# Kernel tuning notes

Hardware: AMD Instinct MI355X
Metric: run time of the kernel (lower is better)

The kernel has to match this reference:

```python
import jax, jax.numpy as jnp
import numpy as np

B, L, D, H = 2, 4096, 768, 12
HS = D // H  # head_size = 64
SCALE = HS ** -0.5


def setup_inputs() -> dict:
    key = jax.random.key(0)
    k1, k2, k3 = jax.random.split(key, 3)
    x = jax.random.normal(k1, (B, L, D), dtype=jnp.float32)
    # torch nn.Linear weights are [out_features, in_features]; y = x @ W.T
    Wq = jax.random.normal(k2, (D, D), dtype=jnp.float32) * (D ** -0.5)
    Wo = jax.random.normal(k3, (D, D), dtype=jnp.float32) * (D ** -0.5)
    return {"x": x, "Wq": Wq, "Wo": Wo}


def reference(x, Wq, Wo):
    b, l, d = x.shape
    # NOTE: source module uses self.query for Q, K, AND V (bug preserved).
    q = jnp.einsum('bld,ed->ble', x, Wq)              # [B,L,D]
    q = q.reshape(b, l, H, HS).transpose(0, 2, 1, 3)   # [B,H,L,HS]
    k = v = q                                          # K = V = Q (faithful)
    scores = jnp.einsum('bhqd,bhkd->bhqk', q, k) * SCALE  # [B,H,L,L]
    attn = jax.nn.softmax(scores, axis=-1)
    out = jnp.einsum('bhqk,bhkd->bhqd', attn, v)       # [B,H,L,HS]
    out = out.transpose(0, 2, 1, 3).reshape(b, l, d)   # [B,L,D]
    out = jnp.einsum('bld,ed->ble', out, Wo)           # output projection
    return out
```

## Files before the change

kernel.cpp:

```cpp
#include <hip/hip_runtime.h>
#include <hip/hip_bf16.h>

#define LQ 4096
#define DQ 768
#define NH 12
#define NB 2

typedef __attribute__((ext_vector_type(8))) short short8;
typedef __attribute__((ext_vector_type(2))) unsigned uint2v;
typedef __attribute__((ext_vector_type(4))) float f32x4;

__device__ __forceinline__ short f2bf(float f) {
    union { float f; unsigned u; } v; v.f = f;
    unsigned r = v.u + 0x7FFFu + ((v.u >> 16) & 1u);
    return (short)(r >> 16);
}

__device__ __forceinline__ unsigned pk2(float a, float b) {
    float2 t; t.x = a; t.y = b;
    __hip_bfloat162 h = __float22bfloat162_rn(t);
    unsigned u; __builtin_memcpy(&u, &h, 4);
    return u;
}

__device__ __forceinline__ f32x4 mfma16(short8 a, short8 b, f32x4 c) {
    return __builtin_amdgcn_mfma_f32_16x16x32_bf16(a, b, c, 0, 0, 0);
}

__device__ __forceinline__ void gld16(const short* g, short* l) {
    __builtin_amdgcn_global_load_lds(
        (const __attribute__((address_space(1))) unsigned int*)(g),
        (__attribute__((address_space(3))) unsigned int*)(l), 16, 0, 0);
}

#define SQRT_C 0.424660891f

__global__ __launch_bounds__(256) void cvtw(const float* __restrict__ a,
                                            short* __restrict__ o) {
    int i = blockIdx.x * 256 + threadIdx.x;
    float4 v = ((const float4*)a)[i];
    *(uint2v*)&o[i * 4] = (uint2v){pk2(v.x, v.y), pk2(v.z, v.w)};
}


template <int MODE>
__global__ __launch_bounds__(256, 3) void gemm_nt(const short* __restrict__ A,
                                                  const short* __restrict__ Wb,
                                                  void* __restrict__ Cp,
                                                  short* __restrict__ Vf) {
    __shared__ __attribute__((aligned(16))) short As[2][128 * 64];
    __shared__ __attribute__((aligned(16))) short Bs[2][64 * 64];
    const int t = threadIdx.x;
    const int lane = t & 63, w = t >> 6;
    const int lr = lane & 15, qd = lane >> 4;
    const int wm = (w & 1) * 64, wn = (w >> 1) * 32;
    const int lin = blockIdx.x;
    const int xcd = lin & 7, jj = lin >> 3;
    const int nt = jj % 12, mt = (jj / 12) * 8 + xcd;
    const int m0 = mt * 128, n0 = nt * 64;

    int aoffs[4], boffs[2];
#pragma unroll
    for (int u = 0; u < 4; ++u) {
        int c = (u * 4 + w) * 64 + lane;
        int row = c >> 3, k = (c & 7) ^ (row & 7);
        aoffs[u] = (m0 + row) * DQ + k * 8;
    }
#pragma unroll
    for (int u = 0; u < 2; ++u) {
        int c = (u * 4 + w) * 64 + lane;
        int row = c >> 3, k = (c & 7) ^ (row & 7);
        boffs[u] = (n0 + row) * DQ + k * 8;
    }

    f32x4 acc[4][2];
#pragma unroll
    for (int i = 0; i < 4; ++i)
#pragma unroll
        for (int j = 0; j < 2; ++j) acc[i][j] = (f32x4){0.f, 0.f, 0.f, 0.f};

#pragma unroll
    for (int u = 0; u < 4; ++u) gld16(&A[aoffs[u]], &As[0][(u * 4 + w) * 512]);
#pragma unroll
    for (int u = 0; u < 2; ++u) gld16(&Wb[boffs[u]], &Bs[0][(u * 4 + w) * 512]);
    __syncthreads();

    int cur = 0;
    for (int kt = 0; kt < 12; ++kt) {
        if (kt < 11) {
            const int k0 = (kt + 1) * 64;
#pragma unroll
            for (int u = 0; u < 4; ++u) gld16(&A[aoffs[u] + k0], &As[cur ^ 1][(u * 4 + w) * 512]);
#pragma unroll
            for (int u = 0; u < 2; ++u) gld16(&Wb[boffs[u] + k0], &Bs[cur ^ 1][(u * 4 + w) * 512]);
        }
#pragma unroll
        for (int s = 0; s < 2; ++s) {
            const int cq = ((4 * s + qd) ^ (lr & 7)) * 8;
            short8 af[4], bf[2];
#pragma unroll
            for (int i = 0; i < 4; ++i)
                af[i] = *(short8*)&As[cur][(wm + 16 * i + lr) * 64 + cq];
#pragma unroll
            for (int j = 0; j < 2; ++j)
                bf[j] = *(short8*)&Bs[cur][(wn + 16 * j + lr) * 64 + cq];
#pragma unroll
            for (int i = 0; i < 4; ++i)
#pragma unroll
                for (int j = 0; j < 2; ++j)
                    acc[i][j] = mfma16(af[i], bf[j], acc[i][j]);
        }
        __syncthreads();
        cur ^= 1;
    }

    if (MODE == 0) {
#pragma unroll
        for (int i = 0; i < 4; ++i)
#pragma unroll
            for (int j = 0; j < 2; ++j) {
                const int row0 = m0 + wm + 16 * i + qd * 4;
                const int col = n0 + wn + 16 * j + lr;
#pragma unroll
                for (int r = 0; r < 4; ++r)
                    ((float*)Cp)[(size_t)(row0 + r) * DQ + col] = acc[i][j][r];
            }
    } else {
        short* Qf = (short*)Cp;
        short* F = (short*)As;
        const int bh = (m0 >> 12) * NH + nt;
        const size_t gbase = (size_t)bh * (LQ * 64) + (size_t)(((m0 & 4095) >> 6) << 12);
#pragma unroll
        for (int i = 0; i < 4; ++i)
#pragma unroll
            for (int j = 0; j < 2; ++j) {
                const int kl = wm + 16 * i + qd * 4;
                const int hs = wn + 16 * j + lr;
                const int fi = ((kl >> 6) << 12) + ((((hs >> 4) << 1) + ((kl >> 5) & 1)) << 9)
                             + (((hs & 15) + (((kl >> 3) & 3) << 4)) << 3) + (kl & 7);
                *(uint2v*)&F[fi] = (uint2v){pk2(acc[i][j][0], acc[i][j][1]),
                                            pk2(acc[i][j][2], acc[i][j][3])};
            }
        __syncthreads();
#pragma unroll
        for (int p = 0; p < 4; ++p) {
            int u = t + 256 * p;
            *(short8*)&Vf[gbase + (size_t)u * 8] = *(short8*)&F[u * 8];
        }
        __syncthreads();
#pragma unroll
        for (int i = 0; i < 4; ++i)
#pragma unroll
            for (int j = 0; j < 2; ++j) {
                const int hs = wn + 16 * j + lr;
#pragma unroll
                for (int r = 0; r < 4; ++r) {
                    const int key = wm + 16 * i + qd * 4 + r;
                    const int fi = ((key >> 6) << 12) + (((((key >> 4) & 3) << 1) + (hs >> 5)) << 9)
                                 + (((qd * 4 + r) + (((hs >> 3) & 3) << 4)) << 3) + (hs & 7);
                    F[fi] = f2bf(acc[i][j][r] * SQRT_C);
                }
            }
        __syncthreads();
#pragma unroll
        for (int p = 0; p < 4; ++p) {
            int u = t + 256 * p;
            *(short8*)&Qf[gbase + (size_t)u * 8] = *(short8*)&F[u * 8];
        }
    }
}

__global__ __launch_bounds__(256, 3) void attn(const short* __restrict__ Qf,
                                               const short* __restrict__ Vf,
                                               short* __restrict__ O) {
    const int linear = blockIdx.x;
    const int xcd = linear & 7, slot = linear >> 3;
    const int bh = 3 * xcd + (slot >> 5);
    const int qtile = slot & 31;
    const int t = threadIdx.x;
    const int lane = t & 63, w = t >> 6;
    const int qw = w & 1, half = w >> 1;
    const int lr = lane & 15, qd = lane >> 4;

    __shared__ alignas(16) char smem[43008];
    short* aqs = (short*)smem;
    short* Ps = (short*)(smem + 16384) + w * 2560;

    const short* Qbh = Qf + (size_t)bh * (LQ * 64);
    const short* Vbh = Vf + (size_t)bh * (LQ * 64);
    const int q0 = qtile * 128 + qw * 64;
    const int kb0 = half * 64;

    const short one_bf = (short)0x3F80;
    short8 ones;
#pragma unroll
    for (int j = 0; j < 8; ++j) ones[j] = one_bf;

#pragma unroll
    for (int p = 0; p < 4; ++p) {
        int off = (t + 256 * p) * 8;
        *(short8*)&aqs[off] = *(const short8*)&Qbh[(size_t)qtile * 8192 + off];
    }
    __syncthreads();

    f32x4 oacc[4][4], lacc[4];
#pragma unroll
    for (int i = 0; i < 4; ++i) {
        lacc[i] = (f32x4){0.f, 0.f, 0.f, 0.f};
#pragma unroll
        for (int t2 = 0; t2 < 4; ++t2) oacc[i][t2] = (f32x4){0.f, 0.f, 0.f, 0.f};
    }

    const int aqbase = qw * 4096 + lane * 8;

    for (int kb = kb0; kb < kb0 + 64; ++kb) {
        short8 kf[2][2];
#pragma unroll
        for (int t4 = 0; t4 < 2; ++t4)
#pragma unroll
            for (int s = 0; s < 2; ++s)
                kf[t4][s] = *(const short8*)&Qbh[kb * 2048 + (t4 * 2 + s) * 512 + lane * 8];

#pragma unroll
        for (int i = 0; i < 4; ++i) {
            short8 aq0 = *(const short8*)&aqs[aqbase + i * 1024];
            short8 aq1 = *(const short8*)&aqs[aqbase + i * 1024 + 512];
            f32x4 s0 = (f32x4){0.f, 0.f, 0.f, 0.f};
            f32x4 s1 = (f32x4){0.f, 0.f, 0.f, 0.f};
            s0 = mfma16(kf[0][0], aq0, s0);
            s0 = mfma16(kf[0][1], aq1, s0);
            s1 = mfma16(kf[1][0], aq0, s1);
            s1 = mfma16(kf[1][1], aq1, s1);
            *(uint2v*)&Ps[i * 640 + lr * 40 + 4 * qd] =
                (uint2v){pk2(__builtin_amdgcn_exp2f(s0[0]), __builtin_amdgcn_exp2f(s0[1])),
                         pk2(__builtin_amdgcn_exp2f(s0[2]), __builtin_amdgcn_exp2f(s0[3]))};
            *(uint2v*)&Ps[i * 640 + lr * 40 + 16 + 4 * qd] =
                (uint2v){pk2(__builtin_amdgcn_exp2f(s1[0]), __builtin_amdgcn_exp2f(s1[1])),
                         pk2(__builtin_amdgcn_exp2f(s1[2]), __builtin_amdgcn_exp2f(s1[3]))};
        }

        short8 vb[4];
#pragma unroll
        for (int t2 = 0; t2 < 4; ++t2)
            vb[t2] = *(const short8*)&Vbh[(kb >> 1) * 4096 + (kb & 1) * 512 + t2 * 1024 + lane * 8];

#pragma unroll
        for (int i = 0; i < 4; ++i) {
            short8 pa = *(short8*)&Ps[i * 640 + lr * 40 + qd * 8];
#pragma unroll
            for (int t2 = 0; t2 < 4; ++t2)
                oacc[i][t2] = mfma16(pa, vb[t2], oacc[i][t2]);
            lacc[i] = mfma16(pa, ones, lacc[i]);
        }
    }

    __syncthreads();
    f32x4* ex = (f32x4*)smem + (qw * 64 + lane) * 21;
    if (half) {
#pragma unroll
        for (int i = 0; i < 4; ++i) {
#pragma unroll
            for (int t2 = 0; t2 < 4; ++t2) ex[i * 4 + t2] = oacc[i][t2];
            ex[16 + i] = lacc[i];
        }
    }
    __syncthreads();
    if (half) return;

#pragma unroll
    for (int i = 0; i < 4; ++i) {
#pragma unroll
        for (int t2 = 0; t2 < 4; ++t2) oacc[i][t2] += ex[i * 4 + t2];
        lacc[i] += ex[16 + i];
    }

    const int b = bh / NH, h = bh % NH;
#pragma unroll
    for (int i = 0; i < 4; ++i) {
        float inv[4];
#pragma unroll
        for (int r = 0; r < 4; ++r) inv[r] = 1.0f / lacc[i][r];
#pragma unroll
        for (int t2 = 0; t2 < 4; ++t2)
#pragma unroll
            for (int r = 0; r < 4; ++r) {
                int lq = q0 + 16 * i + qd * 4 + r;
                int e = h * 64 + 16 * t2 + lr;
                O[((size_t)(b * LQ + lq)) * DQ + e] = f2bf(oacc[i][t2][r] * inv[r]);
            }
    }
}

extern "C" void kernel_launch(void* const* d_in, const int* in_sizes, int n_in,
                              void* d_out, int out_size, void* d_ws, size_t ws_size,
                              hipStream_t stream) {
    (void)in_sizes; (void)n_in; (void)out_size; (void)ws_size;
    const float* x  = (const float*)d_in[0];
    const float* Wq = (const float*)d_in[1];
    const float* Wo = (const float*)d_in[2];
    float* out = (float*)d_out;

    const size_t NQ = (size_t)NB * NH * LQ * 64;
    const size_t NW = (size_t)DQ * DQ;
    short* Qf  = (short*)d_ws;
    short* Vfb = Qf + NQ;
    short* Ows = Vfb + NQ;
    short* Wqb = Ows + (size_t)NB * LQ * DQ;
    short* Wob = Wqb + NW;

    cvtw<<<(NB * LQ * DQ) / 1024, 256, 0, stream>>>(x, Ows);
    cvtw<<<NW / 1024, 256, 0, stream>>>(Wq, Wqb);
    cvtw<<<NW / 1024, 256, 0, stream>>>(Wo, Wob);
    gemm_nt<1><<<768, 256, 0, stream>>>(Ows, Wqb, Qf, Vfb);
    attn<<<768, 256, 0, stream>>>(Qf, Vfb, Ows);
    gemm_nt<0><<<768, 256, 0, stream>>>(Ows, Wob, out, nullptr);
}
```

Measured before the change: 233.4 us.

## Enlarge GEMM tiles to 128x192 with 512-thread blocks

Both projection GEMMs now use 128x192 output tiles computed by 8 waves (512 threads) instead of 128x64 tiles with 4 waves, and the grid shrinks from 768 to 256 blocks. Each A tile is reused across three heads' worth of columns, which cuts redundant global loads of the activation matrix. The Q/V epilogue is reworked to scatter into three heads per block through a single shared buffer. The cost is larger LDS use, fewer blocks than CUs (256 on a 256-CU part), and potentially lower occupancy.

```diff
diff --git a/kernel.cpp b/kernel.cpp
--- a/kernel.cpp
+++ b/kernel.cpp
@@ -44,45 +44,44 @@
 
 
 template <int MODE>
-__global__ __launch_bounds__(256, 3) void gemm_nt(const short* __restrict__ A,
+__global__ __launch_bounds__(512, 2) void gemm_nt(const short* __restrict__ A,
                                                   const short* __restrict__ Wb,
                                                   void* __restrict__ Cp,
                                                   short* __restrict__ Vf) {
-    __shared__ __attribute__((aligned(16))) short As[2][128 * 64];
-    __shared__ __attribute__((aligned(16))) short Bs[2][64 * 64];
+    __shared__ __attribute__((aligned(16))) short smem[40960];
     const int t = threadIdx.x;
     const int lane = t & 63, w = t >> 6;
     const int lr = lane & 15, qd = lane >> 4;
-    const int wm = (w & 1) * 64, wn = (w >> 1) * 32;
+    const int wm = (w >> 2) * 64, wn = (w & 3) * 48;
     const int lin = blockIdx.x;
     const int xcd = lin & 7, jj = lin >> 3;
-    const int nt = jj % 12, mt = (jj / 12) * 8 + xcd;
-    const int m0 = mt * 128, n0 = nt * 64;
-
-    int aoffs[4], boffs[2];
-#pragma unroll
-    for (int u = 0; u < 4; ++u) {
-        int c = (u * 4 + w) * 64 + lane;
+    const int nt = jj & 3, mt = (jj >> 2) * 8 + xcd;
+    const int m0 = mt * 128, n0 = nt * 192;
+
+    int aoffs[2], boffs[3];
+#pragma unroll
+    for (int u = 0; u < 2; ++u) {
+        int c = (u * 8 + w) * 64 + lane;
         int row = c >> 3, k = (c & 7) ^ (row & 7);
         aoffs[u] = (m0 + row) * DQ + k * 8;
     }
 #pragma unroll
-    for (int u = 0; u < 2; ++u) {
-        int c = (u * 4 + w) * 64 + lane;
+    for (int u = 0; u < 3; ++u) {
+        int c = (u * 8 + w) * 64 + lane;
         int row = c >> 3, k = (c & 7) ^ (row & 7);
         boffs[u] = (n0 + row) * DQ + k * 8;
     }
 
-    f32x4 acc[4][2];
+    f32x4 acc[4][3];
 #pragma unroll
     for (int i = 0; i < 4; ++i)
 #pragma unroll
-        for (int j = 0; j < 2; ++j) acc[i][j] = (f32x4){0.f, 0.f, 0.f, 0.f};
-
-#pragma unroll
-    for (int u = 0; u < 4; ++u) gld16(&A[aoffs[u]], &As[0][(u * 4 + w) * 512]);
-#pragma unroll
-    for (int u = 0; u < 2; ++u) gld16(&Wb[boffs[u]], &Bs[0][(u * 4 + w) * 512]);
+        for (int j = 0; j < 3; ++j) acc[i][j] = (f32x4){0.f, 0.f, 0.f, 0.f};
+
+#pragma unroll
+    for (int u = 0; u < 2; ++u) gld16(&A[aoffs[u]], &smem[(u * 8 + w) * 512]);
+#pragma unroll
+    for (int u = 0; u < 3; ++u) gld16(&Wb[boffs[u]], &smem[16384 + (u * 8 + w) * 512]);
     __syncthreads();
 
     int cur = 0;
@@ -90,24 +89,28 @@
         if (kt < 11) {
             const int k0 = (kt + 1) * 64;
 #pragma unroll
-            for (int u = 0; u < 4; ++u) gld16(&A[aoffs[u] + k0], &As[cur ^ 1][(u * 4 + w) * 512]);
-#pragma unroll
-            for (int u = 0; u < 2; ++u) gld16(&Wb[boffs[u] + k0], &Bs[cur ^ 1][(u * 4 + w) * 512]);
-        }
+            for (int u = 0; u < 2; ++u)
+                gld16(&A[aoffs[u] + k0], &smem[(cur ^ 1) * 8192 + (u * 8 + w) * 512]);
+#pragma unroll
+            for (int u = 0; u < 3; ++u)
+                gld16(&Wb[boffs[u] + k0], &smem[16384 + (cur ^ 1) * 12288 + (u * 8 + w) * 512]);
+        }
+        const short* Asb = &smem[cur * 8192];
+        const short* Bsb = &smem[16384 + cur * 12288];
 #pragma unroll
         for (int s = 0; s < 2; ++s) {
             const int cq = ((4 * s + qd) ^ (lr & 7)) * 8;
-            short8 af[4], bf[2];
+            short8 af[4], bf[3];
 #pragma unroll
             for (int i = 0; i < 4; ++i)
-                af[i] = *(short8*)&As[cur][(wm + 16 * i + lr) * 64 + cq];
-#pragma unroll
-            for (int j = 0; j < 2; ++j)
-                bf[j] = *(short8*)&Bs[cur][(wn + 16 * j + lr) * 64 + cq];
+                af[i] = *(const short8*)&Asb[(wm + 16 * i + lr) * 64 + cq];
+#pragma unroll
+            for (int j = 0; j < 3; ++j)
+                bf[j] = *(const short8*)&Bsb[(wn + 16 * j + lr) * 64 + cq];
 #pragma unroll
             for (int i = 0; i < 4; ++i)
 #pragma unroll
-                for (int j = 0; j < 2; ++j)
+                for (int j = 0; j < 3; ++j)
                     acc[i][j] = mfma16(af[i], bf[j], acc[i][j]);
         }
         __syncthreads();
@@ -118,7 +121,7 @@
 #pragma unroll
         for (int i = 0; i < 4; ++i)
 #pragma unroll
-            for (int j = 0; j < 2; ++j) {
+            for (int j = 0; j < 3; ++j) {
                 const int row0 = m0 + wm + 16 * i + qd * 4;
                 const int col = n0 + wn + 16 * j + lr;
 #pragma unroll
@@ -127,45 +130,53 @@
             }
     } else {
         short* Qf = (short*)Cp;
-        short* F = (short*)As;
-        const int bh = (m0 >> 12) * NH + nt;
-        const size_t gbase = (size_t)bh * (LQ * 64) + (size_t)(((m0 & 4095) >> 6) << 12);
+        short* F = smem;
+        const int bh0 = (m0 >> 12) * NH + nt * 3;
+        const int kl0 = m0 & 4095;
 #pragma unroll
         for (int i = 0; i < 4; ++i)
 #pragma unroll
-            for (int j = 0; j < 2; ++j) {
+            for (int j = 0; j < 3; ++j) {
                 const int kl = wm + 16 * i + qd * 4;
-                const int hs = wn + 16 * j + lr;
-                const int fi = ((kl >> 6) << 12) + ((((hs >> 4) << 1) + ((kl >> 5) & 1)) << 9)
+                const int hsg = wn + 16 * j + lr;
+                const int hh = hsg >> 6, hs = hsg & 63;
+                const int fi = hh * 8192 + ((kl >> 6) & 1) * 4096
+                             + ((((hs >> 4) << 1) + ((kl >> 5) & 1)) << 9)
                              + (((hs & 15) + (((kl >> 3) & 3) << 4)) << 3) + (kl & 7);
                 *(uint2v*)&F[fi] = (uint2v){pk2(acc[i][j][0], acc[i][j][1]),
                                             pk2(acc[i][j][2], acc[i][j][3])};
             }
         __syncthreads();
 #pragma unroll
-        for (int p = 0; p < 4; ++p) {
-            int u = t + 256 * p;
-            *(short8*)&Vf[gbase + (size_t)u * 8] = *(short8*)&F[u * 8];
+        for (int p = 0; p < 6; ++p) {
+            int u = t + 512 * p;
+            int hh = u >> 10, rem = u & 1023;
+            size_t g = (size_t)(bh0 + hh) * (LQ * 64) + (size_t)((kl0 >> 6) << 12);
+            *(short8*)&Vf[g + (size_t)rem * 8] = *(short8*)&F[u * 8];
         }
         __syncthreads();
 #pragma unroll
         for (int i = 0; i < 4; ++i)
 #pragma unroll
-            for (int j = 0; j < 2; ++j) {
-                const int hs = wn + 16 * j + lr;
+            for (int j = 0; j < 3; ++j) {
+                const int hsg = wn + 16 * j + lr;
+                const int hh = hsg >> 6, hs = hsg & 63;
 #pragma unroll
                 for (int r = 0; r < 4; ++r) {
                     const int key = wm + 16 * i + qd * 4 + r;
-                    const int fi = ((key >> 6) << 12) + (((((key >> 4) & 3) << 1) + (hs >> 5)) << 9)
+                    const int fi = hh * 8192 + ((key >> 6) & 1) * 4096
+                                 + (((((key >> 4) & 3) << 1) + (hs >> 5)) << 9)
                                  + (((qd * 4 + r) + (((hs >> 3) & 3) << 4)) << 3) + (hs & 7);
                     F[fi] = f2bf(acc[i][j][r] * SQRT_C);
                 }
             }
         __syncthreads();
 #pragma unroll
-        for (int p = 0; p < 4; ++p) {
-            int u = t + 256 * p;
-            *(short8*)&Qf[gbase + (size_t)u * 8] = *(short8*)&F[u * 8];
+        for (int p = 0; p < 6; ++p) {
+            int u = t + 512 * p;
+            int hh = u >> 10, rem = u & 1023;
+            size_t g = (size_t)(bh0 + hh) * (LQ * 64) + (size_t)((kl0 >> 6) << 12);
+            *(short8*)&Qf[g + (size_t)rem * 8] = *(short8*)&F[u * 8];
         }
     }
 }
@@ -311,7 +322,7 @@
     cvtw<<<(NB * LQ * DQ) / 1024, 256, 0, stream>>>(x, Ows);
     cvtw<<<NW / 1024, 256, 0, stream>>>(Wq, Wqb);
     cvtw<<<NW / 1024, 256, 0, stream>>>(Wo, Wob);
-    gemm_nt<1><<<768, 256, 0, stream>>>(Ows, Wqb, Qf, Vfb);
+    gemm_nt<1><<<256, 512, 0, stream>>>(Ows, Wqb, Qf, Vfb);
     attn<<<768, 256, 0, stream>>>(Qf, Vfb, Ows);
-    gemm_nt<0><<<768, 256, 0, stream>>>(Ows, Wob, out, nullptr);
-}
+    gemm_nt<0><<<256, 512, 0, stream>>>(Ows, Wob, out, nullptr);
+}
```

New measurement: 233.3 us. About the same (-0.1%).
